# Kernel tuning notes

Measured on AMD Instinct MI355X. Metric: run time of the kernel, lower is better.

## Reference

```python
import jax, jax.numpy as jnp
import numpy as np
import math

D = 3  # feature dim hardcoded in source


def setup_inputs() -> dict:
    key = jax.random.key(0)
    k1, k2, k3, k4 = jax.random.split(key, 4)
    B, H, S = 4, 8, 2048
    x = jax.random.normal(k1, (B, 1, S, D), dtype=jnp.float32)
    W_query = jax.random.normal(k2, (1, H, D, D), dtype=jnp.float32)
    W_key = jax.random.uniform(k3, (1, H, D, D), dtype=jnp.float32)
    W_value = jax.random.uniform(k4, (1, H, D, D), dtype=jnp.float32)
    return {"x": x, "W_query": W_query, "W_key": W_key, "W_value": W_value}


def reference(x, W_query, W_key, W_value):
    # Q/K/V projections: [B,1,S,d] @ [1,H,d,d] -> [B,H,S,d]
    Q = jnp.einsum('bosd,ohde->bhse', x, W_query)
    K = jnp.einsum('bosd,ohde->bhse', x, W_key)
    V = jnp.einsum('bosd,ohde->bhse', x, W_value)
    scale = 1.0 / math.sqrt(D)
    # scores: [B,H,S,S]
    scores = jnp.einsum('bhqd,bhkd->bhqk', Q, K) * scale
    weights = jax.nn.softmax(scores, axis=-1)
    ctx = jnp.einsum('bhqk,bhkd->bhqd', weights, V)
    # source returns (torch result, flash result) — mathematically identical
    return (ctx, ctx)
```

## Files before the change

kernel.cpp:

```cpp
#include <hip/hip_runtime.h>

#define SEQ 2048
#define NH 8
#define NB 4

typedef unsigned int u32;
typedef short bf16x8_t __attribute__((ext_vector_type(8)));
typedef float f32x16_t __attribute__((ext_vector_type(16)));

__device__ __forceinline__ u32 pkb(float a, float b) {
    const u32 ua = __builtin_bit_cast(u32, a) + 0x8000u;
    const u32 ub = __builtin_bit_cast(u32, b) + 0x8000u;
    return __builtin_amdgcn_perm(ub, ua, 0x07060302u);
}
__device__ __forceinline__ u32 pks(float Fa, float Fb) {
    const u32 ia = (u32)Fa;
    const u32 ib = (u32)Fb;
    return __builtin_amdgcn_perm(ib, ia, 0x07060302u);
}

union UBv { bf16x8_t v; u32 u[4]; };

__global__ __launch_bounds__(256)
void attn_mfma(const float* __restrict__ x, const float* __restrict__ Wq,
               const float* __restrict__ Wk, const float* __restrict__ Wv,
               float* __restrict__ out) {
    __shared__ __align__(16) char VT4[128 * 128];
    __shared__ __align__(16) float RED[2][4][8][16];

    const int tid = threadIdx.x;
    const int blk = blockIdx.x;
    const int qb   = blk & 63;
    const int rest = blk >> 6;
    const int hp   = rest & 3;
    const int b    = rest >> 2;
    const int h0   = hp * 2, h1 = h0 + 1;

    const float* xb = x + b * SEQ * 3;

    const int lane = tid & 63;
    const int wid  = tid >> 6;
    const int ql   = lane & 31;
    const int q    = qb * 32 + ql;
    const int kbase = wid * 512;

    float ax0[16], ax1[16], ax2[16];
#pragma unroll
    for (int t = 0; t < 16; ++t) {
        const float* kp = xb + (kbase + t * 32 + ql) * 3;
        ax0[t] = kp[0]; ax1[t] = kp[1]; ax2[t] = kp[2];
    }

    {
        const float4* xg = (const float4*)xb;
        float xv[24];
        const float4 t0 = xg[tid * 6 + 0]; xv[0]=t0.x; xv[1]=t0.y; xv[2]=t0.z; xv[3]=t0.w;
        const float4 t1 = xg[tid * 6 + 1]; xv[4]=t1.x; xv[5]=t1.y; xv[6]=t1.z; xv[7]=t1.w;
        const float4 t2 = xg[tid * 6 + 2]; xv[8]=t2.x; xv[9]=t2.y; xv[10]=t2.z; xv[11]=t2.w;
        const float4 t3 = xg[tid * 6 + 3]; xv[12]=t3.x; xv[13]=t3.y; xv[14]=t3.z; xv[15]=t3.w;
        const float4 t4 = xg[tid * 6 + 4]; xv[16]=t4.x; xv[17]=t4.y; xv[18]=t4.z; xv[19]=t4.w;
        const float4 t5 = xg[tid * 6 + 5]; xv[20]=t5.x; xv[21]=t5.y; xv[22]=t5.z; xv[23]=t5.w;
        const int kt   = tid >> 1;
        const int half = tid & 1;
        const int slotA = half * 4;
        char* base = VT4 + kt * 128;
#pragma unroll
        for (int d = 0; d < 3; ++d) {
            uint2 wa, wb;
            wa.x = pkb(xv[0 + d],  xv[3 + d]);
            wa.y = pkb(xv[6 + d],  xv[9 + d]);
            wb.x = pkb(xv[12 + d], xv[15 + d]);
            wb.y = pkb(xv[18 + d], xv[21 + d]);
            *(uint2*)(base + d * 32 + slotA * 2)      = wa;
            *(uint2*)(base + d * 32 + slotA * 2 + 16) = wb;
        }
        uint4 ones; ones.x = ones.y = ones.z = ones.w = 0x3F803F80u;
        *(uint4*)(base + 96 + half * 16) = ones;
    }

    u32 A0[16], A1[16];
#pragma unroll
    for (int t = 0; t < 16; ++t) {
        A0[t] = pkb(ax0[t], ax1[t]);
        A1[t] = pkb(ax2[t], 0.f);
    }

    const float* gq = xb + q * 3;
    const float xq0 = gq[0], xq1 = gq[1], xq2 = gq[2];
    const float cc = 0.5773502691896258f * 1.4426950408889634f * 8388608.0f;
    float u00, u01, u02, u10, u11, u12;
    {
        const float* wqp = Wq + h0 * 9; const float* wkp = Wk + h0 * 9;
        const float Q0 = xq0 * wqp[0] + xq1 * wqp[3] + xq2 * wqp[6];
        const float Q1 = xq0 * wqp[1] + xq1 * wqp[4] + xq2 * wqp[7];
        const float Q2 = xq0 * wqp[2] + xq1 * wqp[5] + xq2 * wqp[8];
        u00 = (Q0 * wkp[0] + Q1 * wkp[1] + Q2 * wkp[2]) * cc;
        u01 = (Q0 * wkp[3] + Q1 * wkp[4] + Q2 * wkp[5]) * cc;
        u02 = (Q0 * wkp[6] + Q1 * wkp[7] + Q2 * wkp[8]) * cc;
    }
    {
        const float* wqp = Wq + h1 * 9; const float* wkp = Wk + h1 * 9;
        const float Q0 = xq0 * wqp[0] + xq1 * wqp[3] + xq2 * wqp[6];
        const float Q1 = xq0 * wqp[1] + xq1 * wqp[4] + xq2 * wqp[7];
        const float Q2 = xq0 * wqp[2] + xq1 * wqp[5] + xq2 * wqp[8];
        u10 = (Q0 * wkp[0] + Q1 * wkp[1] + Q2 * wkp[2]) * cc;
        u11 = (Q0 * wkp[3] + Q1 * wkp[4] + Q2 * wkp[5]) * cc;
        u12 = (Q0 * wkp[6] + Q1 * wkp[7] + Q2 * wkp[8]) * cc;
    }

    __syncthreads();

    UBv Bs0, Bs1;
    Bs0.u[0] = (lane < 32) ? pkb(u00, u01) : 0u;
    Bs0.u[1] = (lane < 32) ? pkb(u02, 0.f) : 0u;
    Bs0.u[2] = 0u; Bs0.u[3] = 0u;
    Bs1.u[0] = (lane < 32) ? pkb(u10, u11) : 0u;
    Bs1.u[1] = (lane < 32) ? pkb(u12, 0.f) : 0u;
    Bs1.u[2] = 0u; Bs1.u[3] = 0u;

    const char* vb = VT4 + wid * 4096 + (lane & 3) * 32 + (lane >> 5) * 16;

    f32x16_t bc;
#pragma unroll
    for (int i = 0; i < 16; ++i) bc[i] = 1065353216.0f;

    const int d31 = lane & 31;
    const int slot = ((lane >> 5) << 2) | d31;

#pragma unroll
    for (int head = 0; head < 2; ++head) {
        const UBv Bs = head ? Bs1 : Bs0;
        f32x16_t pvC = {};
#pragma unroll
        for (int t = 0; t < 16; ++t) {
            const uint4 bv0 = *(const uint4*)(vb + t * 256);
            const uint4 bv1 = *(const uint4*)(vb + t * 256 + 128);
            UBv B0; B0.u[0] = bv0.x; B0.u[1] = bv0.y; B0.u[2] = bv0.z; B0.u[3] = bv0.w;
            UBv B1; B1.u[0] = bv1.x; B1.u[1] = bv1.y; B1.u[2] = bv1.z; B1.u[3] = bv1.w;

            UBv A; A.u[0] = A0[t]; A.u[1] = A1[t]; A.u[2] = 0u; A.u[3] = 0u;
            const f32x16_t sc = __builtin_amdgcn_mfma_f32_32x32x16_bf16(A.v, Bs.v, bc, 0, 0, 0);

            UBv PA;
            PA.u[0] = pks(sc[0],  sc[1]);
            PA.u[1] = pks(sc[2],  sc[3]);
            PA.u[2] = pks(sc[4],  sc[5]);
            PA.u[3] = pks(sc[6],  sc[7]);
            pvC = __builtin_amdgcn_mfma_f32_32x32x16_bf16(PA.v, B0.v, pvC, 0, 0, 0);
            UBv PB;
            PB.u[0] = pks(sc[8],  sc[9]);
            PB.u[1] = pks(sc[10], sc[11]);
            PB.u[2] = pks(sc[12], sc[13]);
            PB.u[3] = pks(sc[14], sc[15]);
            pvC = __builtin_amdgcn_mfma_f32_32x32x16_bf16(PB.v, B1.v, pvC, 0, 0, 0);
        }
        if (d31 < 4) {
#pragma unroll
            for (int i = 0; i < 4; ++i) {
                float4 w; w.x = pvC[i*4+0]; w.y = pvC[i*4+1];
                w.z = pvC[i*4+2]; w.w = pvC[i*4+3];
                *(float4*)&RED[head][wid][slot][i * 4] = w;
            }
        }
    }
    __syncthreads();

    if (wid < 2 && lane < 32) {
        const int head = wid;
        const int hh   = head ? h1 : h0;
        const float* wvp = Wv + hh * 9;
        const int qrow = lane;
        const int hh2 = (qrow >> 2) & 1;
        const int r   = (qrow & 3) | ((qrow >> 3) << 2);
        float acc[4];
#pragma unroll
        for (int d = 0; d < 4; ++d)
            acc[d] = (RED[head][0][hh2 * 4 + d][r] + RED[head][1][hh2 * 4 + d][r])
                   + (RED[head][2][hh2 * 4 + d][r] + RED[head][3][hh2 * 4 + d][r]);
        const float inv = 1.0f / fmaxf(acc[3], 1e-37f);
        const float r0 = acc[0] * inv, r1 = acc[1] * inv, r2 = acc[2] * inv;
        const float o0 = r0 * wvp[0] + r1 * wvp[3] + r2 * wvp[6];
        const float o1 = r0 * wvp[1] + r1 * wvp[4] + r2 * wvp[7];
        const float o2 = r0 * wvp[2] + r1 * wvp[5] + r2 * wvp[8];
        const int bhO = b * NH + hh;
        const int o   = bhO * (SEQ * 3) + (qb * 32 + qrow) * 3;
        const int second = NB * NH * SEQ * 3;
        out[o + 0] = o0; out[o + 1] = o1; out[o + 2] = o2;
        out[o + second + 0] = o0; out[o + second + 1] = o1; out[o + second + 2] = o2;
    }
}

extern "C" void kernel_launch(void* const* d_in, const int* in_sizes, int n_in,
                              void* d_out, int out_size, void* d_ws, size_t ws_size,
                              hipStream_t stream) {
    const float* x  = (const float*)d_in[0];
    const float* Wq = (const float*)d_in[1];
    const float* Wk = (const float*)d_in[2];
    const float* Wv = (const float*)d_in[3];
    float* out = (float*)d_out;
    (void)in_sizes; (void)n_in; (void)d_ws; (void)ws_size; (void)out_size;

    const int grid = NB * (NH / 2) * (SEQ / 32);
    attn_mfma<<<grid, 256, 0, stream>>>(x, Wq, Wk, Wv, out);
}
```

Measured before the change: 20.43 us.

## Drop float-to-int converts in exp trick and fuse both heads in one loop

The bit-level exponential approximation now adds a 2^23-offset bias and a 2^7 scale inside the score MFMA accumulator. The bf16 exp bits then land in the low half of the fp32 result and can be taken with a byte permute, so the per-element float-to-uint converts disappear. The two-head loop is merged so each LDS V-tile load and each A operand serves both heads, with two accumulators in flight. The x2 component of the A operand is packed two per register to save VGPRs, at the cost of a shift or mask per step. The bias encoding trades exponent range for this: large scores may wrap in the low mantissa bits.

After: 18.71 us. 1.09x faster.

```diff
diff --git a/kernel.cpp b/kernel.cpp
--- a/kernel.cpp
+++ b/kernel.cpp
@@ -14,9 +14,8 @@
     return __builtin_amdgcn_perm(ub, ua, 0x07060302u);
 }
 __device__ __forceinline__ u32 pks(float Fa, float Fb) {
-    const u32 ia = (u32)Fa;
-    const u32 ib = (u32)Fb;
-    return __builtin_amdgcn_perm(ib, ia, 0x07060302u);
+    return __builtin_amdgcn_perm(__builtin_bit_cast(u32, Fb),
+                                 __builtin_bit_cast(u32, Fa), 0x05040100u);
 }
 
 union UBv { bf16x8_t v; u32 u[4]; };
@@ -78,16 +77,15 @@
         *(uint4*)(base + 96 + half * 16) = ones;
     }
 
-    u32 A0[16], A1[16];
-#pragma unroll
-    for (int t = 0; t < 16; ++t) {
-        A0[t] = pkb(ax0[t], ax1[t]);
-        A1[t] = pkb(ax2[t], 0.f);
-    }
+    u32 A0[16], A1h[8];
+#pragma unroll
+    for (int t = 0; t < 16; ++t) A0[t] = pkb(ax0[t], ax1[t]);
+#pragma unroll
+    for (int j = 0; j < 8; ++j)  A1h[j] = pkb(ax2[2 * j], ax2[2 * j + 1]);
 
     const float* gq = xb + q * 3;
     const float xq0 = gq[0], xq1 = gq[1], xq2 = gq[2];
-    const float cc = 0.5773502691896258f * 1.4426950408889634f * 8388608.0f;
+    const float cc = 0.5773502691896258f * 1.4426950408889634f * 128.0f;
     float u00, u01, u02, u10, u11, u12;
     {
         const float* wqp = Wq + h0 * 9; const float* wkp = Wk + h0 * 9;
@@ -120,47 +118,65 @@
 
     const char* vb = VT4 + wid * 4096 + (lane & 3) * 32 + (lane >> 5) * 16;
 
+    f32x16_t pvC0 = {};
+    f32x16_t pvC1 = {};
     f32x16_t bc;
 #pragma unroll
-    for (int i = 0; i < 16; ++i) bc[i] = 1065353216.0f;
-
-    const int d31 = lane & 31;
-    const int slot = ((lane >> 5) << 2) | d31;
-
-#pragma unroll
-    for (int head = 0; head < 2; ++head) {
-        const UBv Bs = head ? Bs1 : Bs0;
-        f32x16_t pvC = {};
-#pragma unroll
-        for (int t = 0; t < 16; ++t) {
-            const uint4 bv0 = *(const uint4*)(vb + t * 256);
-            const uint4 bv1 = *(const uint4*)(vb + t * 256 + 128);
-            UBv B0; B0.u[0] = bv0.x; B0.u[1] = bv0.y; B0.u[2] = bv0.z; B0.u[3] = bv0.w;
-            UBv B1; B1.u[0] = bv1.x; B1.u[1] = bv1.y; B1.u[2] = bv1.z; B1.u[3] = bv1.w;
-
-            UBv A; A.u[0] = A0[t]; A.u[1] = A1[t]; A.u[2] = 0u; A.u[3] = 0u;
-            const f32x16_t sc = __builtin_amdgcn_mfma_f32_32x32x16_bf16(A.v, Bs.v, bc, 0, 0, 0);
-
+    for (int i = 0; i < 16; ++i) bc[i] = 8404864.0f;
+
+#pragma unroll
+    for (int t = 0; t < 16; ++t) {
+        const uint4 bv0 = *(const uint4*)(vb + t * 256);
+        const uint4 bv1 = *(const uint4*)(vb + t * 256 + 128);
+        UBv B0; B0.u[0] = bv0.x; B0.u[1] = bv0.y; B0.u[2] = bv0.z; B0.u[3] = bv0.w;
+        UBv B1; B1.u[0] = bv1.x; B1.u[1] = bv1.y; B1.u[2] = bv1.z; B1.u[3] = bv1.w;
+
+        UBv A;
+        A.u[0] = A0[t];
+        A.u[1] = (t & 1) ? (A1h[t >> 1] >> 16) : (A1h[t >> 1] & 0xFFFFu);
+        A.u[2] = 0u; A.u[3] = 0u;
+
+        {
+            const f32x16_t sc = __builtin_amdgcn_mfma_f32_32x32x16_bf16(A.v, Bs0.v, bc, 0, 0, 0);
             UBv PA;
             PA.u[0] = pks(sc[0],  sc[1]);
             PA.u[1] = pks(sc[2],  sc[3]);
             PA.u[2] = pks(sc[4],  sc[5]);
             PA.u[3] = pks(sc[6],  sc[7]);
-            pvC = __builtin_amdgcn_mfma_f32_32x32x16_bf16(PA.v, B0.v, pvC, 0, 0, 0);
+            pvC0 = __builtin_amdgcn_mfma_f32_32x32x16_bf16(PA.v, B0.v, pvC0, 0, 0, 0);
             UBv PB;
             PB.u[0] = pks(sc[8],  sc[9]);
             PB.u[1] = pks(sc[10], sc[11]);
             PB.u[2] = pks(sc[12], sc[13]);
             PB.u[3] = pks(sc[14], sc[15]);
-            pvC = __builtin_amdgcn_mfma_f32_32x32x16_bf16(PB.v, B1.v, pvC, 0, 0, 0);
-        }
-        if (d31 < 4) {
-#pragma unroll
-            for (int i = 0; i < 4; ++i) {
-                float4 w; w.x = pvC[i*4+0]; w.y = pvC[i*4+1];
-                w.z = pvC[i*4+2]; w.w = pvC[i*4+3];
-                *(float4*)&RED[head][wid][slot][i * 4] = w;
-            }
+            pvC0 = __builtin_amdgcn_mfma_f32_32x32x16_bf16(PB.v, B1.v, pvC0, 0, 0, 0);
+        }
+        {
+            const f32x16_t sc = __builtin_amdgcn_mfma_f32_32x32x16_bf16(A.v, Bs1.v, bc, 0, 0, 0);
+            UBv PA;
+            PA.u[0] = pks(sc[0],  sc[1]);
+            PA.u[1] = pks(sc[2],  sc[3]);
+            PA.u[2] = pks(sc[4],  sc[5]);
+            PA.u[3] = pks(sc[6],  sc[7]);
+            pvC1 = __builtin_amdgcn_mfma_f32_32x32x16_bf16(PA.v, B0.v, pvC1, 0, 0, 0);
+            UBv PB;
+            PB.u[0] = pks(sc[8],  sc[9]);
+            PB.u[1] = pks(sc[10], sc[11]);
+            PB.u[2] = pks(sc[12], sc[13]);
+            PB.u[3] = pks(sc[14], sc[15]);
+            pvC1 = __builtin_amdgcn_mfma_f32_32x32x16_bf16(PB.v, B1.v, pvC1, 0, 0, 0);
+        }
+    }
+
+    const int d31 = lane & 31;
+    if (d31 < 4) {
+        const int slot = ((lane >> 5) << 2) | d31;
+#pragma unroll
+        for (int i = 0; i < 4; ++i) {
+            float4 w0; w0.x = pvC0[i*4+0]; w0.y = pvC0[i*4+1]; w0.z = pvC0[i*4+2]; w0.w = pvC0[i*4+3];
+            *(float4*)&RED[0][wid][slot][i * 4] = w0;
+            float4 w1; w1.x = pvC1[i*4+0]; w1.y = pvC1[i*4+1]; w1.z = pvC1[i*4+2]; w1.w = pvC1[i*4+3];
+            *(float4*)&RED[1][wid][slot][i * 4] = w1;
         }
     }
     __syncthreads();
```
